# Kernel optimization log

Hardware: AMD Instinct MI355X
Metric: run time of the kernel (lower is better)

## Reference

```python
import jax, jax.numpy as jnp
import numpy as np

LN_EPS = 1e-5

def layer_norm(x, w, b):
    m = jnp.mean(x, axis=-1, keepdims=True)
    v = jnp.mean((x - m) ** 2, axis=-1, keepdims=True)
    return (x - m) * jax.lax.rsqrt(v + LN_EPS) * w + b

def setup_inputs() -> dict:
    key = jax.random.key(0)
    ks = jax.random.split(key, 10)
    B, N, L = 32, 576, 100
    low, high = 1024, 1536
    inp = {
        "vit_feat": jax.random.normal(ks[0], (B, N, low), dtype=jnp.float32),
        "box_feat": jax.random.normal(ks[1], (B, L, high), dtype=jnp.float32),
        "lengths": jax.random.randint(ks[2], (B,), 0, L, dtype=jnp.int64),
        # query projector: LayerNorm(low) + Linear(low, low)
        "q_ln_w": jnp.ones((low,), jnp.float32),
        "q_ln_b": jnp.zeros((low,), jnp.float32),
        "q_w": jax.random.normal(ks[3], (low, low), dtype=jnp.float32) * 0.02,
        "q_b": jnp.zeros((low,), jnp.float32),
        # key projector: LayerNorm(high) + Linear(high, low)
        "k_ln_w": jnp.ones((high,), jnp.float32),
        "k_ln_b": jnp.zeros((high,), jnp.float32),
        "k_w": jax.random.normal(ks[4], (high, low), dtype=jnp.float32) * 0.02,
        "k_b": jnp.zeros((low,), jnp.float32),
        # value projector: LayerNorm(high) + Linear(high, low)
        "v_ln_w": jnp.ones((high,), jnp.float32),
        "v_ln_b": jnp.zeros((high,), jnp.float32),
        "v_w": jax.random.normal(ks[5], (high, low), dtype=jnp.float32) * 0.02,
        "v_b": jnp.zeros((low,), jnp.float32),
    }
    return inp

def reference(vit_feat, box_feat, lengths,
              q_ln_w, q_ln_b, q_w, q_b,
              k_ln_w, k_ln_b, k_w, k_b,
              v_ln_w, v_ln_b, v_w, v_b):
    B, L = box_feat.shape[0], box_feat.shape[1]
    # padding mask, same as the original per-row copy loop
    mask = jnp.arange(L)[None, :] < lengths[:, None]          # [B, L] bool
    q = layer_norm(vit_feat, q_ln_w, q_ln_b) @ q_w + q_b      # [B, N, low]
    k = layer_norm(box_feat, k_ln_w, k_ln_b) @ k_w + k_b      # [B, L, low]
    v = layer_norm(box_feat, v_ln_w, v_ln_b) @ v_w + v_b      # [B, L, low]
    scale = 1.0 / jnp.sqrt(jnp.asarray(k.shape[-1], q.dtype))
    att = jnp.einsum('bnd,bld->bnl', q, k * scale)            # [B, N, L]
    att = jnp.where(mask[:, None, :], att, -jnp.inf)
    att = jnp.nan_to_num(att)  # -inf -> finite min, matching torch nan_to_num
    att = jax.nn.softmax(att, axis=-1)
    out = jnp.einsum('bnl,bld->bnd', att, v)                  # [B, N, low]
    return vit_feat + out
```

## Files before the change

kernel.cpp:

```cpp
#include <hip/hip_runtime.h>
#include <stdint.h>

typedef __attribute__((ext_vector_type(8))) short short8;
typedef __attribute__((ext_vector_type(4))) float f32x4;

#define NEG_FLT_MAX (-3.402823466e38f)

__device__ __forceinline__ unsigned short f2bf(float f) {
  uint32_t u = __float_as_uint(f);
  uint32_t r = (u + 0x7fffu + ((u >> 16) & 1u)) >> 16;
  return (unsigned short)r;
}

__device__ __forceinline__ float bf2f(unsigned short u) {
  return __uint_as_float(((uint32_t)u) << 16);
}

__device__ __forceinline__ void gload16(const void* g, void* l) {
  __builtin_amdgcn_global_load_lds(
      (const __attribute__((address_space(1))) uint32_t*)g,
      (__attribute__((address_space(3))) uint32_t*)l, 16, 0, 0);
}

__global__ void tpv_kernel(const float* __restrict__ src, unsigned short* __restrict__ dst) {
  __shared__ float tile[32][33];
  const int c0 = blockIdx.x * 32;
  const int r0 = blockIdx.y * 32;
  const int tx = threadIdx.x, ty = threadIdx.y;
#pragma unroll
  for (int i = ty; i < 32; i += 8)
    tile[i][tx] = src[(size_t)(r0 + i) * 1024 + (c0 + tx)];
  __syncthreads();
#pragma unroll
  for (int i = ty; i < 32; i += 8)
    dst[(size_t)(c0 + i) * 1536 + (r0 + tx)] = f2bf(tile[tx][i]);
}

__global__ __launch_bounds__(256) void wconv_kernel(
    const float* __restrict__ qw, const float* __restrict__ kw,
    unsigned short* __restrict__ qwb, unsigned short* __restrict__ kwb, float scale) {
  const int idx = blockIdx.x * 256 + threadIdx.x;
  const int QG = 1024 * 1024 / 4;
  if (idx < QG) {
    float4 v = ((const float4*)qw)[idx];
    ushort4 o;
    o.x = f2bf(v.x); o.y = f2bf(v.y); o.z = f2bf(v.z); o.w = f2bf(v.w);
    ((ushort4*)qwb)[idx] = o;
  } else {
    const int j = idx - QG;
    float4 v = ((const float4*)kw)[j];
    ushort4 o;
    o.x = f2bf(v.x * scale); o.y = f2bf(v.y * scale);
    o.z = f2bf(v.z * scale); o.w = f2bf(v.w * scale);
    ((ushort4*)kwb)[j] = o;
  }
}

__global__ __launch_bounds__(256) void wvec_kernel(
    const float* __restrict__ qw, const float* __restrict__ kw,
    const float* __restrict__ qb, const float* __restrict__ kb, float scale,
    float* __restrict__ bias3, float* __restrict__ w4, float* __restrict__ c4) {
  const int wv = threadIdx.x >> 6, l = threadIdx.x & 63;
  const int idx = blockIdx.x;
  float s = 0.f;
  if (idx < 256) {
    const int i = idx * 4 + wv;
    const float* row = qw + (size_t)i * 1024;
#pragma unroll
    for (int s0 = 0; s0 < 1024; s0 += 256) {
      float4 a = *(const float4*)(row + s0 + l * 4);
      float4 b = *(const float4*)(kb + s0 + l * 4);
      s += a.x * b.x + a.y * b.y + a.z * b.z + a.w * b.w;
    }
#pragma unroll
    for (int off = 32; off; off >>= 1) s += __shfl_xor(s, off);
    if (l == 0) bias3[i] = s * scale;
  } else if (idx < 640) {
    const int j = (idx - 256) * 4 + wv;
    const float* row = kw + (size_t)j * 1024;
#pragma unroll
    for (int s0 = 0; s0 < 1024; s0 += 256) {
      float4 a = *(const float4*)(row + s0 + l * 4);
      float4 b = *(const float4*)(qb + s0 + l * 4);
      s += a.x * b.x + a.y * b.y + a.z * b.z + a.w * b.w;
    }
#pragma unroll
    for (int off = 32; off; off >>= 1) s += __shfl_xor(s, off);
    if (l == 0) w4[j] = s * scale;
  } else if (wv == 0) {
#pragma unroll
    for (int s0 = 0; s0 < 1024; s0 += 256) {
      float4 a = *(const float4*)(qb + s0 + l * 4);
      float4 b = *(const float4*)(kb + s0 + l * 4);
      s += a.x * b.x + a.y * b.y + a.z * b.z + a.w * b.w;
    }
#pragma unroll
    for (int off = 32; off; off >>= 1) s += __shfl_xor(s, off);
    if (l == 0) *c4 = s * scale;
  }
}

__device__ __forceinline__ void block_reduce2(float& s, float& ss, float* red) {
#pragma unroll
  for (int off = 32; off > 0; off >>= 1) {
    s += __shfl_xor(s, off);
    ss += __shfl_xor(ss, off);
  }
  const int wave = threadIdx.x >> 6;
  const int lane = threadIdx.x & 63;
  if (lane == 0) { red[wave * 2] = s; red[wave * 2 + 1] = ss; }
  __syncthreads();
  if (threadIdx.x == 0) {
    float a = 0.f, b = 0.f;
    for (int i = 0; i < 4; i++) { a += red[i * 2]; b += red[i * 2 + 1]; }
    red[0] = a; red[1] = b;
  }
  __syncthreads();
  s = red[0]; ss = red[1];
}

__global__ __launch_bounds__(256) void ln_vit_kernel(
    const float* __restrict__ x, const float* __restrict__ w,
    const float* __restrict__ b, unsigned short* __restrict__ out) {
  __shared__ float red[8];
  const int row = blockIdx.x;
  const int t = threadIdx.x;
  const float4 v = ((const float4*)(x + (size_t)row * 1024))[t];
  float s = v.x + v.y + v.z + v.w;
  float ss = v.x * v.x + v.y * v.y + v.z * v.z + v.w * v.w;
  block_reduce2(s, ss, red);
  const float m = s * (1.f / 1024.f);
  const float var = ss * (1.f / 1024.f) - m * m;
  const float rstd = rsqrtf(var + 1e-5f);
  const float4 w4 = ((const float4*)w)[t];
  const float4 b4 = ((const float4*)b)[t];
  ushort4 o;
  o.x = f2bf((v.x - m) * rstd * w4.x + b4.x);
  o.y = f2bf((v.y - m) * rstd * w4.y + b4.y);
  o.z = f2bf((v.z - m) * rstd * w4.z + b4.z);
  o.w = f2bf((v.w - m) * rstd * w4.w + b4.w);
  ((ushort4*)(out + (size_t)row * 1024))[t] = o;
}

__global__ __launch_bounds__(256) void ln_box_kernel(
    const float* __restrict__ x,
    const float* __restrict__ kw, const float* __restrict__ kb,
    const float* __restrict__ vw, const float* __restrict__ vb,
    unsigned short* __restrict__ kn, unsigned short* __restrict__ vn) {
  __shared__ float red[8];
  const int row = blockIdx.x;
  const int t = threadIdx.x;
  const float4* xr = (const float4*)(x + (size_t)row * 1536);
  const float4 a = xr[t];
  float4 c = make_float4(0.f, 0.f, 0.f, 0.f);
  if (t < 128) c = xr[256 + t];
  float s = a.x + a.y + a.z + a.w + c.x + c.y + c.z + c.w;
  float ss = a.x * a.x + a.y * a.y + a.z * a.z + a.w * a.w +
             c.x * c.x + c.y * c.y + c.z * c.z + c.w * c.w;
  block_reduce2(s, ss, red);
  const float m = s * (1.f / 1536.f);
  const float var = ss * (1.f / 1536.f) - m * m;
  const float rstd = rsqrtf(var + 1e-5f);
  {
    const float4 w4 = ((const float4*)kw)[t];
    const float4 b4 = ((const float4*)kb)[t];
    ushort4 o;
    o.x = f2bf((a.x - m) * rstd * w4.x + b4.x);
    o.y = f2bf((a.y - m) * rstd * w4.y + b4.y);
    o.z = f2bf((a.z - m) * rstd * w4.z + b4.z);
    o.w = f2bf((a.w - m) * rstd * w4.w + b4.w);
    ((ushort4*)(kn + (size_t)row * 1536))[t] = o;
    const float4 w4v = ((const float4*)vw)[t];
    const float4 b4v = ((const float4*)vb)[t];
    o.x = f2bf((a.x - m) * rstd * w4v.x + b4v.x);
    o.y = f2bf((a.y - m) * rstd * w4v.y + b4v.y);
    o.z = f2bf((a.z - m) * rstd * w4v.z + b4v.z);
    o.w = f2bf((a.w - m) * rstd * w4v.w + b4v.w);
    ((ushort4*)(vn + (size_t)row * 1536))[t] = o;
  }
  if (t < 128) {
    const int t2 = 256 + t;
    const float4 w4 = ((const float4*)kw)[t2];
    const float4 b4 = ((const float4*)kb)[t2];
    ushort4 o;
    o.x = f2bf((c.x - m) * rstd * w4.x + b4.x);
    o.y = f2bf((c.y - m) * rstd * w4.y + b4.y);
    o.z = f2bf((c.z - m) * rstd * w4.z + b4.z);
    o.w = f2bf((c.w - m) * rstd * w4.w + b4.w);
    ((ushort4*)(kn + (size_t)row * 1536))[t2] = o;
    const float4 w4v = ((const float4*)vw)[t2];
    const float4 b4v = ((const float4*)vb)[t2];
    o.x = f2bf((c.x - m) * rstd * w4v.x + b4v.x);
    o.y = f2bf((c.y - m) * rstd * w4v.y + b4v.y);
    o.z = f2bf((c.z - m) * rstd * w4v.z + b4v.z);
    o.w = f2bf((c.w - m) * rstd * w4v.w + b4v.w);
    ((ushort4*)(vn + (size_t)row * 1536))[t2] = o;
  }
}

__global__ __launch_bounds__(256) void qbk_kernel(
    const unsigned short* __restrict__ kn, const float* __restrict__ w4,
    const float* __restrict__ c4, float* __restrict__ qbk) {
  const int wv = threadIdx.x >> 6, l = threadIdx.x & 63;
  const int row = blockIdx.x * 4 + wv;
  const unsigned short* r = kn + (size_t)row * 1536;
  float s = 0.f;
#pragma unroll
  for (int s0 = 0; s0 < 1536; s0 += 512) {
    short8 v = *(const short8*)(r + s0 + l * 8);
    const float* wp = w4 + s0 + l * 8;
    float4 w0 = *(const float4*)wp;
    float4 w1 = *(const float4*)(wp + 4);
    s += bf2f((unsigned short)v[0]) * w0.x + bf2f((unsigned short)v[1]) * w0.y +
         bf2f((unsigned short)v[2]) * w0.z + bf2f((unsigned short)v[3]) * w0.w +
         bf2f((unsigned short)v[4]) * w1.x + bf2f((unsigned short)v[5]) * w1.y +
         bf2f((unsigned short)v[6]) * w1.z + bf2f((unsigned short)v[7]) * w1.w;
  }
#pragma unroll
  for (int off = 32; off; off >>= 1) s += __shfl_xor(s, off);
  if (l == 0) qbk[row] = s + *c4;
}

__device__ __forceinline__ void gemm_core64(
    const unsigned short* __restrict__ A, int lda, int rowmaxA, int tm0,
    const unsigned short* __restrict__ Bt, int ldb, int rowmaxB, int tn0,
    int K, unsigned short* As, unsigned short* Bs, f32x4 acc[4][4]) {
  const int tid = threadIdx.x;
  const int w = tid >> 6, l = tid & 63;
  const int wr = w >> 1, wc = w & 1;
  const int srow = (w << 4) + (l >> 2);
  const int scol = (l & 3) << 3;
  int ra0 = tm0 + srow;      if (ra0 > rowmaxA) ra0 = rowmaxA;
  int ra1 = tm0 + srow + 64; if (ra1 > rowmaxA) ra1 = rowmaxA;
  int rb0 = tn0 + srow;      if (rb0 > rowmaxB) rb0 = rowmaxB;
  int rb1 = tn0 + srow + 64; if (rb1 > rowmaxB) rb1 = rowmaxB;
  const unsigned short* pa0 = A + (size_t)ra0 * lda + scol;
  const unsigned short* pa1 = A + (size_t)ra1 * lda + scol;
  const unsigned short* pb0 = Bt + (size_t)rb0 * ldb + scol;
  const unsigned short* pb1 = Bt + (size_t)rb1 * ldb + scol;
  unsigned short* la0 = As + (w << 4) * 32;
  unsigned short* la1 = As + ((w << 4) + 64) * 32;
  unsigned short* lb0 = Bs + (w << 4) * 32;
  unsigned short* lb1 = Bs + ((w << 4) + 64) * 32;
  const int foff = ((l & 15) << 5) + ((l >> 4) << 3);
  const unsigned short* fa = As + (wr << 6) * 32 + foff;
  const unsigned short* fb = Bs + (wc << 6) * 32 + foff;
#pragma unroll
  for (int i = 0; i < 4; i++)
#pragma unroll
    for (int j = 0; j < 4; j++) acc[i][j] = (f32x4)0.0f;
  for (int k0 = 0; k0 < K; k0 += 64) {
    gload16(pa0 + k0, la0);
    gload16(pa1 + k0, la1);
    gload16(pb0 + k0, lb0);
    gload16(pb1 + k0, lb1);
    gload16(pa0 + k0 + 32, la0 + 4096);
    gload16(pa1 + k0 + 32, la1 + 4096);
    gload16(pb0 + k0 + 32, lb0 + 4096);
    gload16(pb1 + k0 + 32, lb1 + 4096);
    __syncthreads();
    {
      short8 a[4], b[4];
#pragma unroll
      for (int i = 0; i < 4; i++) a[i] = *(const short8*)(fa + i * 512);
#pragma unroll
      for (int j = 0; j < 4; j++) b[j] = *(const short8*)(fb + j * 512);
#pragma unroll
      for (int i = 0; i < 4; i++)
#pragma unroll
        for (int j = 0; j < 4; j++)
          acc[i][j] = __builtin_amdgcn_mfma_f32_16x16x32_bf16(a[i], b[j], acc[i][j], 0, 0, 0);
    }
    {
      short8 a[4], b[4];
#pragma unroll
      for (int i = 0; i < 4; i++) a[i] = *(const short8*)(fa + 4096 + i * 512);
#pragma unroll
      for (int j = 0; j < 4; j++) b[j] = *(const short8*)(fb + 4096 + j * 512);
#pragma unroll
      for (int i = 0; i < 4; i++)
#pragma unroll
        for (int j = 0; j < 4; j++)
          acc[i][j] = __builtin_amdgcn_mfma_f32_16x16x32_bf16(a[i], b[j], acc[i][j], 0, 0, 0);
    }
    __syncthreads();
  }
}

__global__ __launch_bounds__(256) void gemm_w3_kernel(
    const unsigned short* __restrict__ qwb, const unsigned short* __restrict__ kwb,
    unsigned short* __restrict__ W3) {
  __shared__ unsigned short As[128 * 64];
  __shared__ unsigned short Bs[128 * 64];
  const int tm0 = blockIdx.x * 128, tn0 = blockIdx.y * 128;
  f32x4 acc[4][4];
  gemm_core64(qwb, 1024, 1023, tm0, kwb, 1024, 1535, tn0, 1024, As, Bs, acc);
  const int tid = threadIdx.x;
  const int w = tid >> 6, l = tid & 63;
  const int wr = w >> 1, wc = w & 1;
#pragma unroll
  for (int i = 0; i < 4; i++) {
    const int row0 = tm0 + wr * 64 + i * 16 + (l >> 4) * 4;
#pragma unroll
    for (int j = 0; j < 4; j++) {
      const int col = tn0 + wc * 64 + j * 16 + (l & 15);
#pragma unroll
      for (int r = 0; r < 4; r++)
        W3[(size_t)(row0 + r) * 1536 + col] = f2bf(acc[i][j][r]);
    }
  }
}

__global__ __launch_bounds__(256) void gemm_kv_kernel(
    const unsigned short* __restrict__ kn, const unsigned short* __restrict__ vn,
    const unsigned short* __restrict__ W3, const unsigned short* __restrict__ vwt,
    const float* __restrict__ bias3, const float* __restrict__ vb,
    unsigned short* __restrict__ kq, unsigned short* __restrict__ vT) {
  __shared__ unsigned short As[128 * 64];
  __shared__ unsigned short Bs[128 * 64];
  const int z = blockIdx.z;
  const unsigned short* A = z ? vn : kn;
  const unsigned short* Bt = z ? vwt : W3;
  const float* bias = z ? vb : bias3;
  const int M = 3200, N = 1024, K = 1536;
  const int tm0 = blockIdx.x * 128, tn0 = blockIdx.y * 128;
  f32x4 acc[4][4];
  gemm_core64(A, K, M - 1, tm0, Bt, K, N - 1, tn0, K, As, Bs, acc);
  const int tid = threadIdx.x;
  const int w = tid >> 6, l = tid & 63;
  const int wr = w >> 1, wc = w & 1;
#pragma unroll
  for (int i = 0; i < 4; i++) {
    const int row0 = tm0 + wr * 64 + i * 16 + (l >> 4) * 4;
#pragma unroll
    for (int j = 0; j < 4; j++) {
      const int col = tn0 + wc * 64 + j * 16 + (l & 15);
      const float bv = bias[col];
#pragma unroll
      for (int r = 0; r < 4; r++) {
        const int row = row0 + r;
        const float val = acc[i][j][r] + bv;
        if (!z) {
          kq[(size_t)row * N + col] = f2bf(val);
        } else {
          const int bb = row / 100;
          const int ll = row - bb * 100;
          vT[((size_t)bb * N + col) * 128 + ll] = f2bf(val);
        }
      }
    }
  }
}

__global__ __launch_bounds__(256) void attfused_kernel(
    const unsigned short* __restrict__ qn, const unsigned short* __restrict__ kq,
    const unsigned short* __restrict__ vT, const float* __restrict__ qbk,
    const int* __restrict__ lengths, const float* __restrict__ vit,
    float* __restrict__ out) {
  __shared__ __align__(16) char smem[45824];
  float* Smat = (float*)smem;
  float* invr = (float*)(smem + 28672);
  float* qb_l = (float*)(smem + 28800);
  const int PB = 20480, BV = 29440;

  const int b = blockIdx.y;
  const int tm0 = blockIdx.x * 32;
  const int t = threadIdx.x;
  const int w = t >> 6, l = t & 63;
  const int lo = l & 15, hi = l >> 4;
  if (t < 128) qb_l[t] = (t < 100) ? qbk[b * 100 + t] : 0.f;

  const unsigned short* A = qn + (size_t)b * 576 * 1024;
  const unsigned short* B = kq + (size_t)b * 100 * 1024;
  const int ar = (t & 127) >> 2, ah = t >> 7, ac = (t & 3) << 3;
  const unsigned short* paA = A + (size_t)(tm0 + ar) * 1024 + ah * 32 + ac;
  const unsigned short* pbB[4];
#pragma unroll
  for (int i = 0; i < 4; i++) {
    int rb = (i & 1) * 64 + (t >> 2); if (rb > 99) rb = 99;
    pbB[i] = B + (size_t)rb * 1024 + (i >> 1) * 32 + ((t & 3) << 3);
  }
  const int cw = w << 5;

  f32x4 acc[2][2];
#pragma unroll
  for (int i = 0; i < 2; i++) { acc[i][0] = (f32x4)0.0f; acc[i][1] = (f32x4)0.0f; }

  for (int k0 = 0; k0 < 1024; k0 += 64) {
    gload16(paA + k0, smem + w * 1024);
#pragma unroll
    for (int i = 0; i < 4; i++)
      gload16(pbB[i] + k0, smem + 4096 + i * 4096 + w * 1024);
    __syncthreads();
#pragma unroll
    for (int half = 0; half < 2; half++) {
      short8 a[2], bb[2];
#pragma unroll
      for (int i = 0; i < 2; i++)
        a[i] = *(const short8*)(smem + half * 2048 + (i * 16 + lo) * 64 + hi * 16);
#pragma unroll
      for (int j = 0; j < 2; j++)
        bb[j] = *(const short8*)(smem + 4096 + half * 8192 + (cw + j * 16 + lo) * 64 + hi * 16);
#pragma unroll
      for (int i = 0; i < 2; i++)
#pragma unroll
        for (int j = 0; j < 2; j++)
          acc[i][j] = __builtin_amdgcn_mfma_f32_16x16x32_bf16(a[i], bb[j], acc[i][j], 0, 0, 0);
    }
    __syncthreads();
  }

#pragma unroll
  for (int i = 0; i < 2; i++) {
    const int r0 = i * 16 + hi * 4;
#pragma unroll
    for (int j = 0; j < 2; j++) {
      const int c = cw + j * 16 + lo;
      const float qb = qb_l[c];
#pragma unroll
      for (int rr = 0; rr < 4; rr++) Smat[c * 36 + r0 + rr] = acc[i][j][rr] + qb;
    }
  }
  __syncthreads();

  const int r = t >> 3, g = t & 7;
  const int len = lengths[b];
  float mx = NEG_FLT_MAX;
#pragma unroll
  for (int i = 0; i < 13; i++) {
    const int ll = g * 13 + i;
    if (ll < 100) {
      const float v = (ll < len) ? Smat[ll * 36 + r] : NEG_FLT_MAX;
      mx = fmaxf(mx, v);
    }
  }
  mx = fmaxf(mx, __shfl_xor(mx, 1));
  mx = fmaxf(mx, __shfl_xor(mx, 2));
  mx = fmaxf(mx, __shfl_xor(mx, 4));
  float sum = 0.f;
#pragma unroll
  for (int i = 0; i < 13; i++) {
    const int ll = g * 13 + i;
    if (ll < 100) {
      const float v = (ll < len) ? Smat[ll * 36 + r] : NEG_FLT_MAX;
      const float e = __expf(v - mx);
      Smat[ll * 36 + r] = e;
      sum += e;
    }
  }
  sum += __shfl_xor(sum, 1);
  sum += __shfl_xor(sum, 2);
  sum += __shfl_xor(sum, 4);
  if (g == 0) invr[r] = 1.f / sum;
  __syncthreads();

  {
    const float inv = invr[r];
#pragma unroll
    for (int jj = 0; jj < 4; jj++) {
      const int c0 = g * 16 + jj * 4;
      ushort4 o;
      o.x = (c0 + 0 < 100) ? f2bf(Smat[(c0 + 0) * 36 + r] * inv) : (unsigned short)0;
      o.y = (c0 + 1 < 100) ? f2bf(Smat[(c0 + 1) * 36 + r] * inv) : (unsigned short)0;
      o.z = (c0 + 2 < 100) ? f2bf(Smat[(c0 + 2) * 36 + r] * inv) : (unsigned short)0;
      o.w = (c0 + 3 < 100) ? f2bf(Smat[(c0 + 3) * 36 + r] * inv) : (unsigned short)0;
      const int phys = (r * 256 + g * 32 + jj * 8) ^ ((r & 7) << 4);
      *(ushort4*)(smem + PB + phys) = o;
    }
  }
  __syncthreads();

  const unsigned short* vTb = vT + (size_t)b * 131072;
  const float* vitb = vit + ((size_t)b * 576 + tm0) * 1024;
  float* outb = out + ((size_t)b * 576 + tm0) * 1024;
  const int sBcol = ((t & 15) ^ ((t >> 4) & 7)) << 3;
  for (int nt = 0; nt < 16; ++nt) {
#pragma unroll
    for (int i = 0; i < 4; i++) {
      const int vrow = nt * 64 + i * 16 + (t >> 4);
      gload16(vTb + (size_t)vrow * 128 + sBcol, smem + BV + i * 4096 + w * 1024);
    }
    __syncthreads();
    f32x4 acc2[2];
    acc2[0] = (f32x4)0.0f; acc2[1] = (f32x4)0.0f;
#pragma unroll
    for (int ks = 0; ks < 4; ks++) {
      short8 av[2], bv;
#pragma unroll
      for (int i = 0; i < 2; i++) {
        const int m = i * 16 + lo;
        av[i] = *(const short8*)(smem + PB + ((m * 256 + ks * 64 + hi * 16) ^ ((m & 7) << 4)));
      }
      const int n = (w << 4) + lo;
      bv = *(const short8*)(smem + BV + ((n * 256 + ks * 64 + hi * 16) ^ ((n & 7) << 4)));
      acc2[0] = __builtin_amdgcn_mfma_f32_16x16x32_bf16(av[0], bv, acc2[0], 0, 0, 0);
      acc2[1] = __builtin_amdgcn_mfma_f32_16x16x32_bf16(av[1], bv, acc2[1], 0, 0, 0);
    }
#pragma unroll
    for (int i = 0; i < 2; i++) {
      const int col = (w << 4) + lo;
#pragma unroll
      for (int rr = 0; rr < 4; rr++) {
        const int row = i * 16 + hi * 4 + rr;
        *(float*)(smem + ((row * 256 + col * 4) ^ ((row & 7) << 4))) = acc2[i][rr];
      }
    }
    __syncthreads();
#pragma unroll
    for (int m = 0; m < 2; m++) {
      const int row = m * 16 + (t >> 4);
      const int colb = (t & 15) * 4;
      float4 e = *(const float4*)(smem + ((row * 256 + colb * 4) ^ ((row & 7) << 4)));
      const size_t gidx = (size_t)row * 1024 + nt * 64 + colb;
      float4 vv = *(const float4*)(vitb + gidx);
      e.x += vv.x; e.y += vv.y; e.z += vv.z; e.w += vv.w;
      *(float4*)(outb + gidx) = e;
    }
    __syncthreads();
  }
}

extern "C" void kernel_launch(void* const* d_in, const int* in_sizes, int n_in,
                              void* d_out, int out_size, void* d_ws, size_t ws_size,
                              hipStream_t stream) {
  const float* vit = (const float*)d_in[0];
  const float* box = (const float*)d_in[1];
  const int* lengths = (const int*)d_in[2];
  const float* q_ln_w = (const float*)d_in[3];
  const float* q_ln_b = (const float*)d_in[4];
  const float* q_w = (const float*)d_in[5];
  const float* q_b = (const float*)d_in[6];
  const float* k_ln_w = (const float*)d_in[7];
  const float* k_ln_b = (const float*)d_in[8];
  const float* k_w = (const float*)d_in[9];
  const float* k_b = (const float*)d_in[10];
  const float* v_ln_w = (const float*)d_in[11];
  const float* v_ln_b = (const float*)d_in[12];
  const float* v_w = (const float*)d_in[13];
  const float* v_b = (const float*)d_in[14];
  float* out = (float*)d_out;
  char* ws = (char*)d_ws;

  unsigned short* kn    = (unsigned short*)(ws + 0);
  unsigned short* vn    = (unsigned short*)(ws + 9830400);
  unsigned short* v_wt  = (unsigned short*)(ws + 19660800);
  unsigned short* qwb   = (unsigned short*)(ws + 22806528);
  unsigned short* kwb   = (unsigned short*)(ws + 24903680);
  unsigned short* W3    = (unsigned short*)(ws + 28049408);
  float*          bias3 = (float*)(ws + 31195136);
  float*          w4    = (float*)(ws + 31199232);
  float*          c4    = (float*)(ws + 31207424);
  unsigned short* qn    = (unsigned short*)(ws + 0);
  float*          qbk   = (float*)(ws + 37748736);
  unsigned short* kq    = (unsigned short*)(ws + 37761536);
  unsigned short* vT    = (unsigned short*)(ws + 44315136);

  const float scale = 0.03125f;

  wconv_kernel<<<2560, 256, 0, stream>>>(q_w, k_w, qwb, kwb, scale);
  tpv_kernel<<<dim3(32, 48), dim3(32, 8), 0, stream>>>(v_w, v_wt);
  wvec_kernel<<<641, 256, 0, stream>>>(q_w, k_w, q_b, k_b, scale, bias3, w4, c4);

  ln_box_kernel<<<3200, 256, 0, stream>>>(box, k_ln_w, k_ln_b, v_ln_w, v_ln_b, kn, vn);

  gemm_w3_kernel<<<dim3(8, 12), 256, 0, stream>>>(qwb, kwb, W3);

  qbk_kernel<<<800, 256, 0, stream>>>(kn, w4, c4, qbk);

  gemm_kv_kernel<<<dim3(25, 8, 2), 256, 0, stream>>>(
      kn, vn, W3, v_wt, bias3, v_b, kq, vT);

  ln_vit_kernel<<<18432, 256, 0, stream>>>(vit, q_ln_w, q_ln_b, qn);

  attfused_kernel<<<dim3(18, 32), 256, 0, stream>>>(
      qn, kq, vT, qbk, lengths, vit, out);

  (void)in_sizes; (void)n_in; (void)out_size; (void)ws_size;
}
```

Measured before the change: 162.7 us.

## Fuse weight prep kernels, merge box LN with W3 GEMM, fold vit LayerNorm into attention

Merges the three weight-prep kernels into one launch and the box LayerNorm, W3 GEMM and qbk reduction into a single mid kernel using block-index dispatch. It also removes the separate vit LayerNorm kernel and its bf16 intermediate: attention blocks now compute per-row mean and rstd and normalize fp32 vit tiles while staging A into LDS. This cuts launch count and avoids writing and re-reading the normalized query matrix. In exchange the attention kernel reads the fp32 vit rows twice, and its A tile is loaded synchronously instead of through async LDS copies, which may slow the main loop.

```diff
diff --git a/kernel.cpp b/kernel.cpp
--- a/kernel.cpp
+++ b/kernel.cpp
@@ -12,213 +12,89 @@
   return (unsigned short)r;
 }
 
-__device__ __forceinline__ float bf2f(unsigned short u) {
-  return __uint_as_float(((uint32_t)u) << 16);
-}
-
 __device__ __forceinline__ void gload16(const void* g, void* l) {
   __builtin_amdgcn_global_load_lds(
       (const __attribute__((address_space(1))) uint32_t*)g,
       (__attribute__((address_space(3))) uint32_t*)l, 16, 0, 0);
 }
 
-__global__ void tpv_kernel(const float* __restrict__ src, unsigned short* __restrict__ dst) {
+__global__ __launch_bounds__(256) void prep_kernel(
+    const float* __restrict__ qw, const float* __restrict__ kw,
+    const float* __restrict__ vw, const float* __restrict__ qb,
+    const float* __restrict__ kb, float scale,
+    unsigned short* __restrict__ qwb, unsigned short* __restrict__ kwb,
+    unsigned short* __restrict__ vwt,
+    float* __restrict__ bias3, float* __restrict__ w4, float* __restrict__ c4) {
   __shared__ float tile[32][33];
-  const int c0 = blockIdx.x * 32;
-  const int r0 = blockIdx.y * 32;
-  const int tx = threadIdx.x, ty = threadIdx.y;
-#pragma unroll
-  for (int i = ty; i < 32; i += 8)
-    tile[i][tx] = src[(size_t)(r0 + i) * 1024 + (c0 + tx)];
-  __syncthreads();
-#pragma unroll
-  for (int i = ty; i < 32; i += 8)
-    dst[(size_t)(c0 + i) * 1536 + (r0 + tx)] = f2bf(tile[tx][i]);
-}
-
-__global__ __launch_bounds__(256) void wconv_kernel(
-    const float* __restrict__ qw, const float* __restrict__ kw,
-    unsigned short* __restrict__ qwb, unsigned short* __restrict__ kwb, float scale) {
-  const int idx = blockIdx.x * 256 + threadIdx.x;
-  const int QG = 1024 * 1024 / 4;
-  if (idx < QG) {
-    float4 v = ((const float4*)qw)[idx];
-    ushort4 o;
-    o.x = f2bf(v.x); o.y = f2bf(v.y); o.z = f2bf(v.z); o.w = f2bf(v.w);
-    ((ushort4*)qwb)[idx] = o;
+  const int bid = blockIdx.x;
+  const int t = threadIdx.x;
+  if (bid < 2560) {
+    const int idx = bid * 256 + t;
+    const int QG = 1024 * 1024 / 4;
+    if (idx < QG) {
+      float4 v = ((const float4*)qw)[idx];
+      ushort4 o;
+      o.x = f2bf(v.x); o.y = f2bf(v.y); o.z = f2bf(v.z); o.w = f2bf(v.w);
+      ((ushort4*)qwb)[idx] = o;
+    } else {
+      const int j = idx - QG;
+      float4 v = ((const float4*)kw)[j];
+      ushort4 o;
+      o.x = f2bf(v.x * scale); o.y = f2bf(v.y * scale);
+      o.z = f2bf(v.z * scale); o.w = f2bf(v.w * scale);
+      ((ushort4*)kwb)[j] = o;
+    }
+  } else if (bid < 4096) {
+    const int j = bid - 2560;
+    const int c0 = (j & 31) * 32, r0 = (j >> 5) * 32;
+    const int tx = t & 31, ty = t >> 5;
+#pragma unroll
+    for (int i = ty; i < 32; i += 8)
+      tile[i][tx] = vw[(size_t)(r0 + i) * 1024 + (c0 + tx)];
+    __syncthreads();
+#pragma unroll
+    for (int i = ty; i < 32; i += 8)
+      vwt[(size_t)(c0 + i) * 1536 + (r0 + tx)] = f2bf(tile[tx][i]);
   } else {
-    const int j = idx - QG;
-    float4 v = ((const float4*)kw)[j];
-    ushort4 o;
-    o.x = f2bf(v.x * scale); o.y = f2bf(v.y * scale);
-    o.z = f2bf(v.z * scale); o.w = f2bf(v.w * scale);
-    ((ushort4*)kwb)[j] = o;
-  }
-}
-
-__global__ __launch_bounds__(256) void wvec_kernel(
-    const float* __restrict__ qw, const float* __restrict__ kw,
-    const float* __restrict__ qb, const float* __restrict__ kb, float scale,
-    float* __restrict__ bias3, float* __restrict__ w4, float* __restrict__ c4) {
-  const int wv = threadIdx.x >> 6, l = threadIdx.x & 63;
-  const int idx = blockIdx.x;
-  float s = 0.f;
-  if (idx < 256) {
-    const int i = idx * 4 + wv;
-    const float* row = qw + (size_t)i * 1024;
-#pragma unroll
-    for (int s0 = 0; s0 < 1024; s0 += 256) {
-      float4 a = *(const float4*)(row + s0 + l * 4);
-      float4 b = *(const float4*)(kb + s0 + l * 4);
-      s += a.x * b.x + a.y * b.y + a.z * b.z + a.w * b.w;
-    }
-#pragma unroll
-    for (int off = 32; off; off >>= 1) s += __shfl_xor(s, off);
-    if (l == 0) bias3[i] = s * scale;
-  } else if (idx < 640) {
-    const int j = (idx - 256) * 4 + wv;
-    const float* row = kw + (size_t)j * 1024;
-#pragma unroll
-    for (int s0 = 0; s0 < 1024; s0 += 256) {
-      float4 a = *(const float4*)(row + s0 + l * 4);
-      float4 b = *(const float4*)(qb + s0 + l * 4);
-      s += a.x * b.x + a.y * b.y + a.z * b.z + a.w * b.w;
-    }
-#pragma unroll
-    for (int off = 32; off; off >>= 1) s += __shfl_xor(s, off);
-    if (l == 0) w4[j] = s * scale;
-  } else if (wv == 0) {
-#pragma unroll
-    for (int s0 = 0; s0 < 1024; s0 += 256) {
-      float4 a = *(const float4*)(qb + s0 + l * 4);
-      float4 b = *(const float4*)(kb + s0 + l * 4);
-      s += a.x * b.x + a.y * b.y + a.z * b.z + a.w * b.w;
-    }
-#pragma unroll
-    for (int off = 32; off; off >>= 1) s += __shfl_xor(s, off);
-    if (l == 0) *c4 = s * scale;
-  }
-}
-
-__device__ __forceinline__ void block_reduce2(float& s, float& ss, float* red) {
-#pragma unroll
-  for (int off = 32; off > 0; off >>= 1) {
-    s += __shfl_xor(s, off);
-    ss += __shfl_xor(ss, off);
-  }
-  const int wave = threadIdx.x >> 6;
-  const int lane = threadIdx.x & 63;
-  if (lane == 0) { red[wave * 2] = s; red[wave * 2 + 1] = ss; }
-  __syncthreads();
-  if (threadIdx.x == 0) {
-    float a = 0.f, b = 0.f;
-    for (int i = 0; i < 4; i++) { a += red[i * 2]; b += red[i * 2 + 1]; }
-    red[0] = a; red[1] = b;
-  }
-  __syncthreads();
-  s = red[0]; ss = red[1];
-}
-
-__global__ __launch_bounds__(256) void ln_vit_kernel(
-    const float* __restrict__ x, const float* __restrict__ w,
-    const float* __restrict__ b, unsigned short* __restrict__ out) {
-  __shared__ float red[8];
-  const int row = blockIdx.x;
-  const int t = threadIdx.x;
-  const float4 v = ((const float4*)(x + (size_t)row * 1024))[t];
-  float s = v.x + v.y + v.z + v.w;
-  float ss = v.x * v.x + v.y * v.y + v.z * v.z + v.w * v.w;
-  block_reduce2(s, ss, red);
-  const float m = s * (1.f / 1024.f);
-  const float var = ss * (1.f / 1024.f) - m * m;
-  const float rstd = rsqrtf(var + 1e-5f);
-  const float4 w4 = ((const float4*)w)[t];
-  const float4 b4 = ((const float4*)b)[t];
-  ushort4 o;
-  o.x = f2bf((v.x - m) * rstd * w4.x + b4.x);
-  o.y = f2bf((v.y - m) * rstd * w4.y + b4.y);
-  o.z = f2bf((v.z - m) * rstd * w4.z + b4.z);
-  o.w = f2bf((v.w - m) * rstd * w4.w + b4.w);
-  ((ushort4*)(out + (size_t)row * 1024))[t] = o;
-}
-
-__global__ __launch_bounds__(256) void ln_box_kernel(
-    const float* __restrict__ x,
-    const float* __restrict__ kw, const float* __restrict__ kb,
-    const float* __restrict__ vw, const float* __restrict__ vb,
-    unsigned short* __restrict__ kn, unsigned short* __restrict__ vn) {
-  __shared__ float red[8];
-  const int row = blockIdx.x;
-  const int t = threadIdx.x;
-  const float4* xr = (const float4*)(x + (size_t)row * 1536);
-  const float4 a = xr[t];
-  float4 c = make_float4(0.f, 0.f, 0.f, 0.f);
-  if (t < 128) c = xr[256 + t];
-  float s = a.x + a.y + a.z + a.w + c.x + c.y + c.z + c.w;
-  float ss = a.x * a.x + a.y * a.y + a.z * a.z + a.w * a.w +
-             c.x * c.x + c.y * c.y + c.z * c.z + c.w * c.w;
-  block_reduce2(s, ss, red);
-  const float m = s * (1.f / 1536.f);
-  const float var = ss * (1.f / 1536.f) - m * m;
-  const float rstd = rsqrtf(var + 1e-5f);
-  {
-    const float4 w4 = ((const float4*)kw)[t];
-    const float4 b4 = ((const float4*)kb)[t];
-    ushort4 o;
-    o.x = f2bf((a.x - m) * rstd * w4.x + b4.x);
-    o.y = f2bf((a.y - m) * rstd * w4.y + b4.y);
-    o.z = f2bf((a.z - m) * rstd * w4.z + b4.z);
-    o.w = f2bf((a.w - m) * rstd * w4.w + b4.w);
-    ((ushort4*)(kn + (size_t)row * 1536))[t] = o;
-    const float4 w4v = ((const float4*)vw)[t];
-    const float4 b4v = ((const float4*)vb)[t];
-    o.x = f2bf((a.x - m) * rstd * w4v.x + b4v.x);
-    o.y = f2bf((a.y - m) * rstd * w4v.y + b4v.y);
-    o.z = f2bf((a.z - m) * rstd * w4v.z + b4v.z);
-    o.w = f2bf((a.w - m) * rstd * w4v.w + b4v.w);
-    ((ushort4*)(vn + (size_t)row * 1536))[t] = o;
-  }
-  if (t < 128) {
-    const int t2 = 256 + t;
-    const float4 w4 = ((const float4*)kw)[t2];
-    const float4 b4 = ((const float4*)kb)[t2];
-    ushort4 o;
-    o.x = f2bf((c.x - m) * rstd * w4.x + b4.x);
-    o.y = f2bf((c.y - m) * rstd * w4.y + b4.y);
-    o.z = f2bf((c.z - m) * rstd * w4.z + b4.z);
-    o.w = f2bf((c.w - m) * rstd * w4.w + b4.w);
-    ((ushort4*)(kn + (size_t)row * 1536))[t2] = o;
-    const float4 w4v = ((const float4*)vw)[t2];
-    const float4 b4v = ((const float4*)vb)[t2];
-    o.x = f2bf((c.x - m) * rstd * w4v.x + b4v.x);
-    o.y = f2bf((c.y - m) * rstd * w4v.y + b4v.y);
-    o.z = f2bf((c.z - m) * rstd * w4v.z + b4v.z);
-    o.w = f2bf((c.w - m) * rstd * w4v.w + b4v.w);
-    ((ushort4*)(vn + (size_t)row * 1536))[t2] = o;
-  }
-}
-
-__global__ __launch_bounds__(256) void qbk_kernel(
-    const unsigned short* __restrict__ kn, const float* __restrict__ w4,
-    const float* __restrict__ c4, float* __restrict__ qbk) {
-  const int wv = threadIdx.x >> 6, l = threadIdx.x & 63;
-  const int row = blockIdx.x * 4 + wv;
-  const unsigned short* r = kn + (size_t)row * 1536;
-  float s = 0.f;
-#pragma unroll
-  for (int s0 = 0; s0 < 1536; s0 += 512) {
-    short8 v = *(const short8*)(r + s0 + l * 8);
-    const float* wp = w4 + s0 + l * 8;
-    float4 w0 = *(const float4*)wp;
-    float4 w1 = *(const float4*)(wp + 4);
-    s += bf2f((unsigned short)v[0]) * w0.x + bf2f((unsigned short)v[1]) * w0.y +
-         bf2f((unsigned short)v[2]) * w0.z + bf2f((unsigned short)v[3]) * w0.w +
-         bf2f((unsigned short)v[4]) * w1.x + bf2f((unsigned short)v[5]) * w1.y +
-         bf2f((unsigned short)v[6]) * w1.z + bf2f((unsigned short)v[7]) * w1.w;
-  }
-#pragma unroll
-  for (int off = 32; off; off >>= 1) s += __shfl_xor(s, off);
-  if (l == 0) qbk[row] = s + *c4;
+    const int idx = bid - 4096;
+    const int wv = t >> 6, l = t & 63;
+    float s = 0.f;
+    if (idx < 256) {
+      const int i = idx * 4 + wv;
+      const float* row = qw + (size_t)i * 1024;
+#pragma unroll
+      for (int s0 = 0; s0 < 1024; s0 += 256) {
+        float4 a = *(const float4*)(row + s0 + l * 4);
+        float4 b = *(const float4*)(kb + s0 + l * 4);
+        s += a.x * b.x + a.y * b.y + a.z * b.z + a.w * b.w;
+      }
+#pragma unroll
+      for (int off = 32; off; off >>= 1) s += __shfl_xor(s, off);
+      if (l == 0) bias3[i] = s * scale;
+    } else if (idx < 640) {
+      const int j = (idx - 256) * 4 + wv;
+      const float* row = kw + (size_t)j * 1024;
+#pragma unroll
+      for (int s0 = 0; s0 < 1024; s0 += 256) {
+        float4 a = *(const float4*)(row + s0 + l * 4);
+        float4 b = *(const float4*)(qb + s0 + l * 4);
+        s += a.x * b.x + a.y * b.y + a.z * b.z + a.w * b.w;
+      }
+#pragma unroll
+      for (int off = 32; off; off >>= 1) s += __shfl_xor(s, off);
+      if (l == 0) w4[j] = s * scale;
+    } else if (wv == 0) {
+#pragma unroll
+      for (int s0 = 0; s0 < 1024; s0 += 256) {
+        float4 a = *(const float4*)(qb + s0 + l * 4);
+        float4 b = *(const float4*)(kb + s0 + l * 4);
+        s += a.x * b.x + a.y * b.y + a.z * b.z + a.w * b.w;
+      }
+#pragma unroll
+      for (int off = 32; off; off >>= 1) s += __shfl_xor(s, off);
+      if (l == 0) *c4 = s * scale;
+    }
+  }
 }
 
 __device__ __forceinline__ void gemm_core64(
@@ -287,26 +163,109 @@
   }
 }
 
-__global__ __launch_bounds__(256) void gemm_w3_kernel(
+__global__ __launch_bounds__(256) void mid_kernel(
+    const float* __restrict__ box,
+    const float* __restrict__ klnw, const float* __restrict__ klnb,
+    const float* __restrict__ vlnw, const float* __restrict__ vlnb,
     const unsigned short* __restrict__ qwb, const unsigned short* __restrict__ kwb,
-    unsigned short* __restrict__ W3) {
+    const float* __restrict__ w4v, const float* __restrict__ c4,
+    unsigned short* __restrict__ kn, unsigned short* __restrict__ vn,
+    unsigned short* __restrict__ W3, float* __restrict__ qbk) {
+  __shared__ float red[8];
+  __shared__ float redq[4];
   __shared__ unsigned short As[128 * 64];
   __shared__ unsigned short Bs[128 * 64];
-  const int tm0 = blockIdx.x * 128, tn0 = blockIdx.y * 128;
-  f32x4 acc[4][4];
-  gemm_core64(qwb, 1024, 1023, tm0, kwb, 1024, 1535, tn0, 1024, As, Bs, acc);
-  const int tid = threadIdx.x;
-  const int w = tid >> 6, l = tid & 63;
-  const int wr = w >> 1, wc = w & 1;
-#pragma unroll
-  for (int i = 0; i < 4; i++) {
-    const int row0 = tm0 + wr * 64 + i * 16 + (l >> 4) * 4;
-#pragma unroll
-    for (int j = 0; j < 4; j++) {
-      const int col = tn0 + wc * 64 + j * 16 + (l & 15);
-#pragma unroll
-      for (int r = 0; r < 4; r++)
-        W3[(size_t)(row0 + r) * 1536 + col] = f2bf(acc[i][j][r]);
+  const int t = threadIdx.x;
+  if (blockIdx.x < 3200) {
+    const int row = blockIdx.x;
+    const float4* xr = (const float4*)(box + (size_t)row * 1536);
+    const float4 a = xr[t];
+    float4 c = make_float4(0.f, 0.f, 0.f, 0.f);
+    if (t < 128) c = xr[256 + t];
+    float s = a.x + a.y + a.z + a.w + c.x + c.y + c.z + c.w;
+    float ss = a.x * a.x + a.y * a.y + a.z * a.z + a.w * a.w +
+               c.x * c.x + c.y * c.y + c.z * c.z + c.w * c.w;
+#pragma unroll
+    for (int off = 32; off > 0; off >>= 1) {
+      s += __shfl_xor(s, off);
+      ss += __shfl_xor(ss, off);
+    }
+    if ((t & 63) == 0) { red[(t >> 6) * 2] = s; red[(t >> 6) * 2 + 1] = ss; }
+    __syncthreads();
+    if (t == 0) {
+      float aa = 0.f, bb = 0.f;
+      for (int i = 0; i < 4; i++) { aa += red[i * 2]; bb += red[i * 2 + 1]; }
+      red[0] = aa; red[1] = bb;
+    }
+    __syncthreads();
+    s = red[0]; ss = red[1];
+    const float m = s * (1.f / 1536.f);
+    const float var = ss * (1.f / 1536.f) - m * m;
+    const float rstd = rsqrtf(var + 1e-5f);
+    float qd;
+    {
+      const float4 w4 = ((const float4*)klnw)[t];
+      const float4 b4 = ((const float4*)klnb)[t];
+      const float k0v = (a.x - m) * rstd * w4.x + b4.x;
+      const float k1v = (a.y - m) * rstd * w4.y + b4.y;
+      const float k2v = (a.z - m) * rstd * w4.z + b4.z;
+      const float k3v = (a.w - m) * rstd * w4.w + b4.w;
+      ushort4 o;
+      o.x = f2bf(k0v); o.y = f2bf(k1v); o.z = f2bf(k2v); o.w = f2bf(k3v);
+      ((ushort4*)(kn + (size_t)row * 1536))[t] = o;
+      const float4 wq = ((const float4*)w4v)[t];
+      qd = k0v * wq.x + k1v * wq.y + k2v * wq.z + k3v * wq.w;
+      const float4 w4vv = ((const float4*)vlnw)[t];
+      const float4 b4vv = ((const float4*)vlnb)[t];
+      o.x = f2bf((a.x - m) * rstd * w4vv.x + b4vv.x);
+      o.y = f2bf((a.y - m) * rstd * w4vv.y + b4vv.y);
+      o.z = f2bf((a.z - m) * rstd * w4vv.z + b4vv.z);
+      o.w = f2bf((a.w - m) * rstd * w4vv.w + b4vv.w);
+      ((ushort4*)(vn + (size_t)row * 1536))[t] = o;
+    }
+    if (t < 128) {
+      const int t2 = 256 + t;
+      const float4 w4 = ((const float4*)klnw)[t2];
+      const float4 b4 = ((const float4*)klnb)[t2];
+      const float k0v = (c.x - m) * rstd * w4.x + b4.x;
+      const float k1v = (c.y - m) * rstd * w4.y + b4.y;
+      const float k2v = (c.z - m) * rstd * w4.z + b4.z;
+      const float k3v = (c.w - m) * rstd * w4.w + b4.w;
+      ushort4 o;
+      o.x = f2bf(k0v); o.y = f2bf(k1v); o.z = f2bf(k2v); o.w = f2bf(k3v);
+      ((ushort4*)(kn + (size_t)row * 1536))[t2] = o;
+      const float4 wq = ((const float4*)w4v)[t2];
+      qd += k0v * wq.x + k1v * wq.y + k2v * wq.z + k3v * wq.w;
+      const float4 w4vv = ((const float4*)vlnw)[t2];
+      const float4 b4vv = ((const float4*)vlnb)[t2];
+      o.x = f2bf((c.x - m) * rstd * w4vv.x + b4vv.x);
+      o.y = f2bf((c.y - m) * rstd * w4vv.y + b4vv.y);
+      o.z = f2bf((c.z - m) * rstd * w4vv.z + b4vv.z);
+      o.w = f2bf((c.w - m) * rstd * w4vv.w + b4vv.w);
+      ((ushort4*)(vn + (size_t)row * 1536))[t2] = o;
+    }
+#pragma unroll
+    for (int off = 32; off; off >>= 1) qd += __shfl_xor(qd, off);
+    if ((t & 63) == 0) redq[t >> 6] = qd;
+    __syncthreads();
+    if (t == 0) qbk[row] = redq[0] + redq[1] + redq[2] + redq[3] + c4[0];
+  } else {
+    const int j = blockIdx.x - 3200;
+    const int tm0 = (j & 7) * 128, tn0 = (j >> 3) * 128;
+    f32x4 acc[4][4];
+    gemm_core64(qwb, 1024, 1023, tm0, kwb, 1024, 1535, tn0, 1024, As, Bs, acc);
+    const int w = t >> 6, l = t & 63;
+    const int wr = w >> 1, wc = w & 1;
+#pragma unroll
+    for (int i = 0; i < 4; i++) {
+      const int row0 = tm0 + wr * 64 + i * 16 + (l >> 4) * 4;
+#pragma unroll
+      for (int jj = 0; jj < 4; jj++) {
+        const int col = tn0 + wc * 64 + jj * 16 + (l & 15);
+#pragma unroll
+        for (int r = 0; r < 4; r++)
+          W3[(size_t)(row0 + r) * 1536 + col] = f2bf(acc[i][jj][r]);
+      }
     }
   }
 }
@@ -353,14 +312,17 @@
 }
 
 __global__ __launch_bounds__(256) void attfused_kernel(
-    const unsigned short* __restrict__ qn, const unsigned short* __restrict__ kq,
+    const float* __restrict__ vit, const unsigned short* __restrict__ kq,
     const unsigned short* __restrict__ vT, const float* __restrict__ qbk,
-    const int* __restrict__ lengths, const float* __restrict__ vit,
+    const int* __restrict__ lengths,
+    const float* __restrict__ qlnw, const float* __restrict__ qlnb,
     float* __restrict__ out) {
-  __shared__ __align__(16) char smem[45824];
+  __shared__ __align__(16) char smem[46080];
   float* Smat = (float*)smem;
   float* invr = (float*)(smem + 28672);
   float* qb_l = (float*)(smem + 28800);
+  float* rowm = (float*)(smem + 45824);
+  float* rowr = (float*)(smem + 45952);
   const int PB = 20480, BV = 29440;
 
   const int b = blockIdx.y;
@@ -368,26 +330,69 @@
   const int t = threadIdx.x;
   const int w = t >> 6, l = t & 63;
   const int lo = l & 15, hi = l >> 4;
+  const int cw = w << 5;
+  const float* vitb = vit + ((size_t)b * 576 + tm0) * 1024;
+
   if (t < 128) qb_l[t] = (t < 100) ? qbk[b * 100 + t] : 0.f;
-
-  const unsigned short* A = qn + (size_t)b * 576 * 1024;
+  {
+    const int sr2 = t >> 3, g2 = t & 7;
+    const float* vrow = vitb + (size_t)sr2 * 1024 + g2 * 128;
+    float s = 0.f, ss = 0.f;
+#pragma unroll
+    for (int i = 0; i < 32; i++) {
+      float4 v = ((const float4*)vrow)[i];
+      s += v.x + v.y + v.z + v.w;
+      ss += v.x * v.x + v.y * v.y + v.z * v.z + v.w * v.w;
+    }
+    s += __shfl_xor(s, 1); ss += __shfl_xor(ss, 1);
+    s += __shfl_xor(s, 2); ss += __shfl_xor(ss, 2);
+    s += __shfl_xor(s, 4); ss += __shfl_xor(ss, 4);
+    if (g2 == 0) {
+      const float m = s * (1.f / 1024.f);
+      const float var = ss * (1.f / 1024.f) - m * m;
+      rowm[sr2] = m;
+      rowr[sr2] = rsqrtf(var + 1e-5f);
+    }
+  }
+  __syncthreads();
+
   const unsigned short* B = kq + (size_t)b * 100 * 1024;
-  const int ar = (t & 127) >> 2, ah = t >> 7, ac = (t & 3) << 3;
-  const unsigned short* paA = A + (size_t)(tm0 + ar) * 1024 + ah * 32 + ac;
+  const int ar = (t & 127) >> 2;
+  const int cb = (t >> 7) * 32 + ((t & 3) << 3);
+  const float* vitA = vitb + (size_t)ar * 1024 + cb;
+  const float* wA = qlnw + cb;
+  const float* bA = qlnb + cb;
+  const float mA = rowm[ar], rA = rowr[ar];
   const unsigned short* pbB[4];
 #pragma unroll
   for (int i = 0; i < 4; i++) {
     int rb = (i & 1) * 64 + (t >> 2); if (rb > 99) rb = 99;
     pbB[i] = B + (size_t)rb * 1024 + (i >> 1) * 32 + ((t & 3) << 3);
   }
-  const int cw = w << 5;
 
   f32x4 acc[2][2];
 #pragma unroll
   for (int i = 0; i < 2; i++) { acc[i][0] = (f32x4)0.0f; acc[i][1] = (f32x4)0.0f; }
 
   for (int k0 = 0; k0 < 1024; k0 += 64) {
-    gload16(paA + k0, smem + w * 1024);
+    {
+      float4 x0 = *(const float4*)(vitA + k0);
+      float4 x1 = *(const float4*)(vitA + k0 + 4);
+      float4 w0 = *(const float4*)(wA + k0);
+      float4 w1 = *(const float4*)(wA + k0 + 4);
+      float4 b0 = *(const float4*)(bA + k0);
+      float4 b1 = *(const float4*)(bA + k0 + 4);
+      short8 pk;
+      pk[0] = (short)f2bf((x0.x - mA) * rA * w0.x + b0.x);
+      pk[1] = (short)f2bf((x0.y - mA) * rA * w0.y + b0.y);
+      pk[2] = (short)f2bf((x0.z - mA) * rA * w0.z + b0.z);
+      pk[3] = (short)f2bf((x0.w - mA) * rA * w0.w + b0.w);
+      pk[4] = (short)f2bf((x1.x - mA) * rA * w1.x + b1.x);
+      pk[5] = (short)f2bf((x1.y - mA) * rA * w1.y + b1.y);
+      pk[6] = (short)f2bf((x1.z - mA) * rA * w1.z + b1.z);
+      pk[7] = (short)f2bf((x1.w - mA) * rA * w1.w + b1.w);
+      *(short8*)(smem + t * 16) = pk;
+    }
 #pragma unroll
     for (int i = 0; i < 4; i++)
       gload16(pbB[i] + k0, smem + 4096 + i * 4096 + w * 1024);
@@ -471,7 +476,6 @@
   __syncthreads();
 
   const unsigned short* vTb = vT + (size_t)b * 131072;
-  const float* vitb = vit + ((size_t)b * 576 + tm0) * 1024;
   float* outb = out + ((size_t)b * 576 + tm0) * 1024;
   const int sBcol = ((t & 15) ^ ((t >> 4) & 7)) << 3;
   for (int nt = 0; nt < 16; ++nt) {
@@ -550,30 +554,23 @@
   float*          bias3 = (float*)(ws + 31195136);
   float*          w4    = (float*)(ws + 31199232);
   float*          c4    = (float*)(ws + 31207424);
-  unsigned short* qn    = (unsigned short*)(ws + 0);
   float*          qbk   = (float*)(ws + 37748736);
   unsigned short* kq    = (unsigned short*)(ws + 37761536);
   unsigned short* vT    = (unsigned short*)(ws + 44315136);
 
   const float scale = 0.03125f;
 
-  wconv_kernel<<<2560, 256, 0, stream>>>(q_w, k_w, qwb, kwb, scale);
-  tpv_kernel<<<dim3(32, 48), dim3(32, 8), 0, stream>>>(v_w, v_wt);
-  wvec_kernel<<<641, 256, 0, stream>>>(q_w, k_w, q_b, k_b, scale, bias3, w4, c4);
-
-  ln_box_kernel<<<3200, 256, 0, stream>>>(box, k_ln_w, k_ln_b, v_ln_w, v_ln_b, kn, vn);
-
-  gemm_w3_kernel<<<dim3(8, 12), 256, 0, stream>>>(qwb, kwb, W3);
-
-  qbk_kernel<<<800, 256, 0, stream>>>(kn, w4, c4, qbk);
+  prep_kernel<<<4737, 256, 0, stream>>>(q_w, k_w, v_w, q_b, k_b, scale,
+                                        qwb, kwb, v_wt, bias3, w4, c4);
+
+  mid_kernel<<<3296, 256, 0, stream>>>(box, k_ln_w, k_ln_b, v_ln_w, v_ln_b,
+                                       qwb, kwb, w4, c4, kn, vn, W3, qbk);
 
   gemm_kv_kernel<<<dim3(25, 8, 2), 256, 0, stream>>>(
       kn, vn, W3, v_wt, bias3, v_b, kq, vT);
 
-  ln_vit_kernel<<<18432, 256, 0, stream>>>(vit, q_ln_w, q_ln_b, qn);
-
   attfused_kernel<<<dim3(18, 32), 256, 0, stream>>>(
-      qn, kq, vT, qbk, lengths, vit, out);
+      vit, kq, vT, qbk, lengths, q_ln_w, q_ln_b, out);
 
   (void)in_sizes; (void)n_in; (void)out_size; (void)ws_size;
 }
```

After: 154.3 us. 1.05x faster.
